# Kernel optimization log

Measured on AMD Instinct MI355X. Metric: run time of the kernel, lower is better.

## Reference

```python
import jax, jax.numpy as jnp
import numpy as np

N = 500_000      # nodes
E = 1_500_000    # edges (avg degree ~3, AIG-like)
F_IN = 4         # node feature dim
H = 32           # hidden dim fixed by module
S = 7            # state feature dim
BN_EPS = 1e-5


def setup_inputs():
    key = jax.random.key(0)
    ks = jax.random.split(key, 32)
    rn = lambda k, shape, s=0.1: jax.random.normal(k, shape, dtype=jnp.float32) * s
    inp = {}
    inp["states"] = rn(ks[0], (S,), 1.0)
    inp["x"] = rn(ks[1], (N, F_IN), 1.0)
    inp["edge_index"] = jax.random.randint(ks[2], (2, E), 0, N, dtype=jnp.int32)
    inp["edge_attr"] = rn(ks[3], (E, 1), 1.0)
    inp["batch"] = jnp.zeros((N,), dtype=jnp.int32)  # single graph
    dims = [F_IN, H, H]
    for i, (d, k0) in enumerate(zip(dims, [4, 10, 16]), start=1):
        inp[f"eps{i}"] = jnp.zeros((1,), jnp.float32)
        inp[f"elw{i}"] = rn(ks[k0], (d,))            # edge lin: Linear(1, d)
        inp[f"elb{i}"] = jnp.zeros((d,), jnp.float32)
        inp[f"w{i}"] = rn(ks[k0 + 1], (d, H))
        inp[f"b{i}"] = jnp.zeros((H,), jnp.float32)
        inp[f"g{i}"] = jnp.ones((H,), jnp.float32)   # BN gamma
        inp[f"bt{i}"] = jnp.zeros((H,), jnp.float32) # BN beta
    inp["sw"] = rn(ks[22], (S, 16))
    inp["sb"] = jnp.zeros((16,), jnp.float32)
    inp["a1w"] = rn(ks[23], (H + 16, H))
    inp["a1b"] = jnp.zeros((H,), jnp.float32)
    inp["a2w"] = rn(ks[24], (H, 6))
    inp["a2b"] = jnp.zeros((6,), jnp.float32)
    return inp


def _bn(h, g, b):
    # BatchNorm1d over node dim (training-mode batch statistics)
    mu = h.mean(0)
    var = h.var(0)
    return (h - mu) * jax.lax.rsqrt(var + BN_EPS) * g + b


def _gine(x, src, dst, edge_attr, eps, elw, elb, w, b, g, bt):
    # GINEConv: nn((1+eps)*x_i + sum_j relu(x_j + lin(e_ij)))
    e = edge_attr * elw[None, :] + elb                  # [E, d]
    m = jax.nn.relu(x[src] + e)                          # gather + edge-add + relu
    agg = jax.ops.segment_sum(m, dst, num_segments=x.shape[0])  # scatter-sum
    h = (1.0 + eps) * x + agg
    return jax.nn.relu(_bn(h @ w + b, g, bt))


def reference(states, x, edge_index, edge_attr, batch,
              eps1, elw1, elb1, w1, b1, g1, bt1,
              eps2, elw2, elb2, w2, b2, g2, bt2,
              eps3, elw3, elb3, w3, b3, g3, bt3,
              sw, sb, a1w, a1b, a2w, a2b):
    src, dst = edge_index[0], edge_index[1]
    h = _gine(x, src, dst, edge_attr, eps1, elw1, elb1, w1, b1, g1, bt1)
    h = _gine(h, src, dst, edge_attr, eps2, elw2, elb2, w2, b2, g2, bt2)
    h = _gine(h, src, dst, edge_attr, eps3, elw3, elb3, w3, b3, g3, bt3)
    # (global mean/max pooling in the torch forward only feeds the cached
    #  value-head input, not the returned actor output -> omitted here)
    state_x = jax.nn.relu(states @ sw + sb)              # [16]
    a = jnp.concatenate([h, jnp.broadcast_to(state_x, (h.shape[0], 16))], axis=1)
    a = jax.nn.relu(a @ a1w + a1b)
    logits = a @ a2w + a2b                               # [N, num_actions]
    return jax.nn.softmax(logits, axis=-1)               # global_softmax=False
```

## Files before the change

kernel.cpp:

```cpp
#include <hip/hip_runtime.h>
#include <hip/hip_fp16.h>
#include <math.h>

#define TPB 256
#define SCAN_CHUNK 1024
#define NBLK_LAYER 2048
#define NGROUPS (NBLK_LAYER * 8)
#define NBLK_TEAM 2048

struct alignas(16) half8 { __half h[8]; };

__global__ __launch_bounds__(256) void prep_kernel(
    const float* __restrict__ states, const float* __restrict__ sw,
    const float* __restrict__ sb, const float* __restrict__ a1w,
    const float* __restrict__ a1b, float* __restrict__ stats,
    float* __restrict__ c2, int zcount) {
  int t = threadIdx.x;
  for (int j = t; j < zcount; j += 256) stats[j] = 0.0f;
  __shared__ float sx[16];
  if (t < 16) {
    float acc = sb[t];
#pragma unroll
    for (int k = 0; k < 7; ++k) acc += states[k] * sw[k * 16 + t];
    sx[t] = fmaxf(acc, 0.0f);
  }
  __syncthreads();
  if (t < 32) {
    float acc = a1b[t];
#pragma unroll
    for (int k = 0; k < 16; ++k) acc += sx[k] * a1w[(32 + k) * 32 + t];
    c2[t] = acc;
  }
}

__global__ __launch_bounds__(256) void hist3_k(const int* __restrict__ dst,
                                               int* __restrict__ cnt, int E,
                                               int N) {
  int team = blockIdx.x & 7;
  int member = blockIdx.x >> 3;
  int n8 = (N + 7) >> 3;
  int lo = team * n8;
  int hi = lo + n8 < N ? lo + n8 : N;
  int stride = (NBLK_TEAM >> 3) * TPB;
  for (int e = member * TPB + threadIdx.x; e < E; e += stride) {
    int d = dst[e];
    if (d >= lo && d < hi) atomicAdd(&cnt[d], 1);
  }
}

__global__ __launch_bounds__(256) void scan1_k(const int* __restrict__ cnt,
                                               int* __restrict__ pre,
                                               int* __restrict__ bsum, int N) {
  __shared__ int lds[256];
  int b = blockIdx.x, t = threadIdx.x;
  int base = b * SCAN_CHUNK + t * 4;
  int c0 = (base + 0 < N) ? cnt[base + 0] : 0;
  int c1 = (base + 1 < N) ? cnt[base + 1] : 0;
  int c2 = (base + 2 < N) ? cnt[base + 2] : 0;
  int c3 = (base + 3 < N) ? cnt[base + 3] : 0;
  int s = c0 + c1 + c2 + c3;
  lds[t] = s;
  __syncthreads();
  int val = s;
  for (int off = 1; off < 256; off <<= 1) {
    int add = (t >= off) ? lds[t - off] : 0;
    __syncthreads();
    val += add;
    lds[t] = val;
    __syncthreads();
  }
  int excl = val - s;
  if (base + 0 < N) pre[base + 0] = excl;
  if (base + 1 < N) pre[base + 1] = excl + c0;
  if (base + 2 < N) pre[base + 2] = excl + c0 + c1;
  if (base + 3 < N) pre[base + 3] = excl + c0 + c1 + c2;
  if (t == 255) bsum[b] = val;
}

__global__ __launch_bounds__(512) void scan2_k(int* __restrict__ bsum, int nb) {
  __shared__ int lds[512];
  int t = threadIdx.x;
  int v = (t < nb) ? bsum[t] : 0;
  lds[t] = v;
  __syncthreads();
  int val = v;
  for (int off = 1; off < 512; off <<= 1) {
    int add = (t >= off) ? lds[t - off] : 0;
    __syncthreads();
    val += add;
    lds[t] = val;
    __syncthreads();
  }
  if (t < nb) bsum[t] = val - v;
}

__global__ __launch_bounds__(256) void scan3_k(int* __restrict__ pre,
                                               int* __restrict__ cursor,
                                               const int* __restrict__ bsum,
                                               int N, int E) {
  int i = blockIdx.x * TPB + threadIdx.x;
  if (i == 0) pre[N] = E;
  if (i >= N) return;
  int v = pre[i] + bsum[i >> 10];
  pre[i] = v;
  cursor[i] = v;
}

__global__ __launch_bounds__(256) void scatter3_k(
    const int* __restrict__ src, const int* __restrict__ dst,
    const float* __restrict__ ea, int* __restrict__ cursor,
    int2* __restrict__ pe, int E, int N) {
  int team = blockIdx.x & 7;
  int member = blockIdx.x >> 3;
  int n8 = (N + 7) >> 3;
  int lo = team * n8;
  int hi = lo + n8 < N ? lo + n8 : N;
  int stride = (NBLK_TEAM >> 3) * TPB;
  for (int e = member * TPB + threadIdx.x; e < E; e += stride) {
    int d = dst[e];
    if (d >= lo && d < hi) {
      int p = atomicAdd(&cursor[d], 1);
      pe[p] = make_int2(src[e], __float_as_int(ea[e]));
    }
  }
}

__global__ __launch_bounds__(256) void layer1_k(
    const int* __restrict__ rowptr, const int2* __restrict__ pe,
    const float* __restrict__ x, const float* __restrict__ elw,
    const float* __restrict__ elb, const float* __restrict__ w,
    const float* __restrict__ b, const float* __restrict__ epsp,
    __half* __restrict__ zh, float* __restrict__ ostats, int N) {
  const int tid = threadIdx.x;
  const int c = tid & 31;
  const int group0 = blockIdx.x * 8 + (tid >> 5);
  float wc0 = w[0 * 32 + c], wc1 = w[1 * 32 + c], wc2 = w[2 * 32 + c],
        wc3 = w[3 * 32 + c];
  float bc = b[c];
  float w0 = elw[0], w1 = elw[1], w2 = elw[2], w3 = elw[3];
  float e0 = elb[0], e1 = elb[1], e2 = elb[2], e3 = elb[3];
  float one_eps = 1.0f + epsp[0];
  float sl = 0.f, sq = 0.f;
  for (int i = group0; i < N; i += NGROUPS) {
    int p0 = rowptr[i], p1 = rowptr[i + 1];
    float a0 = 0.f, a1 = 0.f, a2 = 0.f, a3 = 0.f;
    for (int p = p0 + c; p < p1; p += 32) {
      int2 e = pe[p];
      float a = __int_as_float(e.y);
      float4 xv = *reinterpret_cast<const float4*>(x + (size_t)e.x * 4);
      a0 += fmaxf(xv.x + fmaf(a, w0, e0), 0.f);
      a1 += fmaxf(xv.y + fmaf(a, w1, e1), 0.f);
      a2 += fmaxf(xv.z + fmaf(a, w2, e2), 0.f);
      a3 += fmaxf(xv.w + fmaf(a, w3, e3), 0.f);
    }
#pragma unroll
    for (int off = 16; off; off >>= 1) {
      a0 += __shfl_xor(a0, off, 32);
      a1 += __shfl_xor(a1, off, 32);
      a2 += __shfl_xor(a2, off, 32);
      a3 += __shfl_xor(a3, off, 32);
    }
    float4 xv = *reinterpret_cast<const float4*>(x + (size_t)i * 4);
    float h0 = fmaf(one_eps, xv.x, a0);
    float h1 = fmaf(one_eps, xv.y, a1);
    float h2 = fmaf(one_eps, xv.z, a2);
    float h3 = fmaf(one_eps, xv.w, a3);
    float zv = bc;
    zv = fmaf(h0, wc0, zv);
    zv = fmaf(h1, wc1, zv);
    zv = fmaf(h2, wc2, zv);
    zv = fmaf(h3, wc3, zv);
    zh[(size_t)i * 32 + c] = __float2half(zv);
    sl += zv;
    sq = fmaf(zv, zv, sq);
  }
  __shared__ float rs[256], rq[256];
  rs[tid] = sl;
  rq[tid] = sq;
  __syncthreads();
  if (tid < 32) {
    float a = 0.f, qq = 0.f;
#pragma unroll
    for (int g = 0; g < 8; ++g) {
      a += rs[g * 32 + tid];
      qq += rq[g * 32 + tid];
    }
    int slot = blockIdx.x & 7;
    atomicAdd(&ostats[slot * 32 + tid], a);
    atomicAdd(&ostats[256 + slot * 32 + tid], qq);
  }
}

__global__ __launch_bounds__(256) void layerH_k(
    const int* __restrict__ rowptr, const int2* __restrict__ pe,
    const __half* __restrict__ zprev, const float* __restrict__ pstats,
    const float* __restrict__ pg, const float* __restrict__ pbt,
    const float* __restrict__ elw, const float* __restrict__ elb,
    const float* __restrict__ w, const float* __restrict__ b,
    const float* __restrict__ epsp, __half* __restrict__ zh,
    float* __restrict__ ostats, int N) {
  const int tid = threadIdx.x;
  const int c = tid & 31;
  const int gib = tid >> 5;
  const int group0 = blockIdx.x * 8 + gib;
  float ps = 0.f, pq = 0.f;
#pragma unroll
  for (int s = 0; s < 8; ++s) {
    ps += pstats[s * 32 + c];
    pq += pstats[256 + s * 32 + c];
  }
  float mu = ps / (float)N;
  float var = pq / (float)N - mu * mu;
  float scale = rsqrtf(var + 1e-5f) * pg[c];
  float shift = pbt[c] - mu * scale;
  float wcol[32];
#pragma unroll
  for (int k = 0; k < 32; ++k) wcol[k] = w[k * 32 + c];
  float elwc = elw[c], elbc = elb[c], bc = b[c];
  float one_eps = 1.0f + epsp[0];
  float sl = 0.f, sq = 0.f;
  __shared__ float hlds[256];
  for (int i = group0; i < N; i += NGROUPS) {
    int p0 = rowptr[i], p1 = rowptr[i + 1];
    float hself =
        fmaxf(fmaf(scale, __half2float(zprev[(size_t)i * 32 + c]), shift), 0.f);
    float acc = 0.f;
    for (int p = p0; p < p1; ++p) {
      int2 e = pe[p];
      float hs = fmaxf(
          fmaf(scale, __half2float(zprev[(size_t)e.x * 32 + c]), shift), 0.f);
      acc += fmaxf(hs + fmaf(__int_as_float(e.y), elwc, elbc), 0.f);
    }
    float hh = fmaf(one_eps, hself, acc);
    hlds[tid] = hh;
    float zv = bc;
    const float4* hp = reinterpret_cast<const float4*>(&hlds[gib * 32]);
#pragma unroll
    for (int kk = 0; kk < 8; ++kk) {
      float4 h4 = hp[kk];
      zv = fmaf(h4.x, wcol[kk * 4 + 0], zv);
      zv = fmaf(h4.y, wcol[kk * 4 + 1], zv);
      zv = fmaf(h4.z, wcol[kk * 4 + 2], zv);
      zv = fmaf(h4.w, wcol[kk * 4 + 3], zv);
    }
    zh[(size_t)i * 32 + c] = __float2half(zv);
    sl += zv;
    sq = fmaf(zv, zv, sq);
  }
  __shared__ float rs[256], rq[256];
  rs[tid] = sl;
  rq[tid] = sq;
  __syncthreads();
  if (tid < 32) {
    float a = 0.f, qq = 0.f;
#pragma unroll
    for (int g = 0; g < 8; ++g) {
      a += rs[g * 32 + tid];
      qq += rq[g * 32 + tid];
    }
    int slot = blockIdx.x & 7;
    atomicAdd(&ostats[slot * 32 + tid], a);
    atomicAdd(&ostats[256 + slot * 32 + tid], qq);
  }
}

__global__ __launch_bounds__(256) void head_k(
    const __half* __restrict__ zh, const float* __restrict__ pstats,
    const float* __restrict__ pg, const float* __restrict__ pbt,
    const float* __restrict__ a1w, const float* __restrict__ c2,
    const float* __restrict__ a2w, const float* __restrict__ a2b,
    float* __restrict__ out, int N) {
  const int tid = threadIdx.x;
  const int c = tid & 31;
  const int gib = tid >> 5;
  const int group0 = blockIdx.x * 8 + gib;
  float ps = 0.f, pq = 0.f;
#pragma unroll
  for (int s = 0; s < 8; ++s) {
    ps += pstats[s * 32 + c];
    pq += pstats[256 + s * 32 + c];
  }
  float mu = ps / (float)N;
  float var = pq / (float)N - mu * mu;
  float scale = rsqrtf(var + 1e-5f) * pg[c];
  float shift = pbt[c] - mu * scale;
  float wcol[32];
#pragma unroll
  for (int k = 0; k < 32; ++k) wcol[k] = a1w[k * 32 + c];
  float c2c = c2[c];
  const int j = c & 7;
  const int g = c >> 3;
  float w2r[8];
#pragma unroll
  for (int u = 0; u < 8; ++u)
    w2r[u] = (j < 6) ? a2w[(8 * g + u) * 6 + j] : 0.f;
  float bj = (j < 6) ? a2b[j] : 0.f;
  __shared__ float ylds[256];
  __shared__ float alds[256];
  __shared__ float llds[64];
  for (int i = group0; i < N; i += NGROUPS) {
    float y =
        fmaxf(fmaf(scale, __half2float(zh[(size_t)i * 32 + c]), shift), 0.f);
    ylds[tid] = y;
    float a1 = c2c;
    const float4* yp = reinterpret_cast<const float4*>(&ylds[gib * 32]);
#pragma unroll
    for (int kk = 0; kk < 8; ++kk) {
      float4 y4 = yp[kk];
      a1 = fmaf(y4.x, wcol[kk * 4 + 0], a1);
      a1 = fmaf(y4.y, wcol[kk * 4 + 1], a1);
      a1 = fmaf(y4.z, wcol[kk * 4 + 2], a1);
      a1 = fmaf(y4.w, wcol[kk * 4 + 3], a1);
    }
    a1 = fmaxf(a1, 0.f);
    alds[tid] = a1;
    const float4* ap =
        reinterpret_cast<const float4*>(&alds[gib * 32 + g * 8]);
    float4 a4a = ap[0];
    float4 a4b = ap[1];
    float l = a4a.x * w2r[0];
    l = fmaf(a4a.y, w2r[1], l);
    l = fmaf(a4a.z, w2r[2], l);
    l = fmaf(a4a.w, w2r[3], l);
    l = fmaf(a4b.x, w2r[4], l);
    l = fmaf(a4b.y, w2r[5], l);
    l = fmaf(a4b.z, w2r[6], l);
    l = fmaf(a4b.w, w2r[7], l);
    l += __shfl_xor(l, 8, 32);
    l += __shfl_xor(l, 16, 32);
    l += bj;
    llds[gib * 8 + j] = l;
    const float4* lp = reinterpret_cast<const float4*>(&llds[gib * 8]);
    float4 L0 = lp[0];
    float4 L1 = lp[1];
    float mx =
        fmaxf(fmaxf(fmaxf(L0.x, L0.y), fmaxf(L0.z, L0.w)), fmaxf(L1.x, L1.y));
    float e0 = __expf(L0.x - mx), e1 = __expf(L0.y - mx),
          e2 = __expf(L0.z - mx), e3 = __expf(L0.w - mx),
          e4 = __expf(L1.x - mx), e5 = __expf(L1.y - mx);
    float inv = 1.0f / (e0 + e1 + e2 + e3 + e4 + e5);
    if (c < 6) {
      float v = e0;
      v = (c == 1) ? e1 : v;
      v = (c == 2) ? e2 : v;
      v = (c == 3) ? e3 : v;
      v = (c == 4) ? e4 : v;
      v = (c == 5) ? e5 : v;
      out[(size_t)i * 6 + c] = v * inv;
    }
  }
}

__global__ __launch_bounds__(256) void edge_d4(
    const int* __restrict__ src, const int* __restrict__ dst,
    const float* __restrict__ ea, const float* __restrict__ x,
    const float* __restrict__ elw, const float* __restrict__ elb,
    float* __restrict__ agg, int E) {
  int e = blockIdx.x * TPB + threadIdx.x;
  if (e >= E) return;
  int s = src[e], d = dst[e];
  float a = ea[e];
  float4 xv = *reinterpret_cast<const float4*>(x + (size_t)s * 4);
  float m0 = fmaxf(xv.x + a * elw[0] + elb[0], 0.0f);
  float m1 = fmaxf(xv.y + a * elw[1] + elb[1], 0.0f);
  float m2 = fmaxf(xv.z + a * elw[2] + elb[2], 0.0f);
  float m3 = fmaxf(xv.w + a * elw[3] + elb[3], 0.0f);
  float* ap = agg + (size_t)d * 32;
  atomicAdd(ap + 0, m0);
  atomicAdd(ap + 1, m1);
  atomicAdd(ap + 2, m2);
  atomicAdd(ap + 3, m3);
}

__global__ __launch_bounds__(256) void edge_d32(
    const int* __restrict__ src, const int* __restrict__ dst,
    const float* __restrict__ ea, const float* __restrict__ x,
    const float* __restrict__ elw, const float* __restrict__ elb,
    float* __restrict__ agg, int E) {
  int tid = blockIdx.x * TPB + threadIdx.x;
  int e = tid >> 5;
  int c = tid & 31;
  if (e >= E) return;
  int s = src[e], d = dst[e];
  float a = ea[e];
  float m = fmaxf(x[(size_t)s * 32 + c] + a * elw[c] + elb[c], 0.0f);
  atomicAdd(agg + (size_t)d * 32 + c, m);
}

template <int DIN>
__global__ __launch_bounds__(256) void node_a(
    const float* __restrict__ x, float* aggz, const float* __restrict__ w,
    const float* __restrict__ b, const float* __restrict__ epsp,
    float* __restrict__ ssum, float* __restrict__ ssq, int N) {
  int i = blockIdx.x * TPB + threadIdx.x;
  float zv[32];
  if (i < N) {
    float one_eps = 1.0f + epsp[0];
    float h[DIN];
    if constexpr (DIN == 4) {
      float4 xv = *reinterpret_cast<const float4*>(x + (size_t)i * 4);
      float4 av = *reinterpret_cast<const float4*>(aggz + (size_t)i * 32);
      h[0] = one_eps * xv.x + av.x;
      h[1] = one_eps * xv.y + av.y;
      h[2] = one_eps * xv.z + av.z;
      h[3] = one_eps * xv.w + av.w;
    } else {
#pragma unroll
      for (int k0 = 0; k0 < 32; k0 += 4) {
        float4 xv = *reinterpret_cast<const float4*>(x + (size_t)i * 32 + k0);
        float4 av =
            *reinterpret_cast<const float4*>(aggz + (size_t)i * 32 + k0);
        h[k0 + 0] = one_eps * xv.x + av.x;
        h[k0 + 1] = one_eps * xv.y + av.y;
        h[k0 + 2] = one_eps * xv.z + av.z;
        h[k0 + 3] = one_eps * xv.w + av.w;
      }
    }
#pragma unroll
    for (int c = 0; c < 32; ++c) zv[c] = b[c];
#pragma unroll
    for (int k = 0; k < DIN; ++k)
#pragma unroll
      for (int c = 0; c < 32; ++c) zv[c] = fmaf(h[k], w[k * 32 + c], zv[c]);
#pragma unroll
    for (int c0 = 0; c0 < 32; c0 += 4) {
      float4 o = make_float4(zv[c0], zv[c0 + 1], zv[c0 + 2], zv[c0 + 3]);
      *reinterpret_cast<float4*>(aggz + (size_t)i * 32 + c0) = o;
    }
  } else {
#pragma unroll
    for (int c = 0; c < 32; ++c) zv[c] = 0.0f;
  }
  __shared__ float ls[32], lq[32];
  if (threadIdx.x < 32) {
    ls[threadIdx.x] = 0.0f;
    lq[threadIdx.x] = 0.0f;
  }
  __syncthreads();
#pragma unroll
  for (int c = 0; c < 32; ++c) {
    float v = zv[c];
    float q = zv[c] * zv[c];
#pragma unroll
    for (int off = 32; off > 0; off >>= 1) {
      v += __shfl_xor(v, off, 64);
      q += __shfl_xor(q, off, 64);
    }
    if ((threadIdx.x & 63) == 0) {
      atomicAdd(&ls[c], v);
      atomicAdd(&lq[c], q);
    }
  }
  __syncthreads();
  if (threadIdx.x < 32) {
    atomicAdd(&ssum[threadIdx.x], ls[threadIdx.x]);
    atomicAdd(&ssq[threadIdx.x], lq[threadIdx.x]);
  }
}

__global__ __launch_bounds__(256) void node_b(
    const float* __restrict__ z, const float* __restrict__ ssum,
    const float* __restrict__ ssq, const float* __restrict__ g,
    const float* __restrict__ bt, float* __restrict__ out, int N) {
  __shared__ float sscale[32], sshift[32];
  if (threadIdx.x < 32) {
    int c = threadIdx.x;
    float mu = ssum[c] / (float)N;
    float var = ssq[c] / (float)N - mu * mu;
    float inv = 1.0f / sqrtf(var + 1e-5f);
    float sc = inv * g[c];
    sscale[c] = sc;
    sshift[c] = bt[c] - mu * sc;
  }
  __syncthreads();
  int i = blockIdx.x * TPB + threadIdx.x;
  if (i >= N) return;
#pragma unroll
  for (int c0 = 0; c0 < 32; c0 += 4) {
    float4 zv = *reinterpret_cast<const float4*>(z + (size_t)i * 32 + c0);
    float4 o;
    o.x = fmaxf(zv.x * sscale[c0 + 0] + sshift[c0 + 0], 0.0f);
    o.y = fmaxf(zv.y * sscale[c0 + 1] + sshift[c0 + 1], 0.0f);
    o.z = fmaxf(zv.z * sscale[c0 + 2] + sshift[c0 + 2], 0.0f);
    o.w = fmaxf(zv.w * sscale[c0 + 3] + sshift[c0 + 3], 0.0f);
    *reinterpret_cast<float4*>(out + (size_t)i * 32 + c0) = o;
  }
}

__global__ __launch_bounds__(256) void node_b3_head(
    const float* __restrict__ z, const float* __restrict__ ssum,
    const float* __restrict__ ssq, const float* __restrict__ g,
    const float* __restrict__ bt, const float* __restrict__ a1w,
    const float* __restrict__ c2, const float* __restrict__ a2w,
    const float* __restrict__ a2b, float* __restrict__ out, int N) {
  __shared__ float sscale[32], sshift[32];
  if (threadIdx.x < 32) {
    int c = threadIdx.x;
    float mu = ssum[c] / (float)N;
    float var = ssq[c] / (float)N - mu * mu;
    float inv = 1.0f / sqrtf(var + 1e-5f);
    float sc = inv * g[c];
    sscale[c] = sc;
    sshift[c] = bt[c] - mu * sc;
  }
  __syncthreads();
  int i = blockIdx.x * TPB + threadIdx.x;
  if (i >= N) return;
  float y[32];
#pragma unroll
  for (int c0 = 0; c0 < 32; c0 += 4) {
    float4 zv = *reinterpret_cast<const float4*>(z + (size_t)i * 32 + c0);
    y[c0 + 0] = fmaxf(zv.x * sscale[c0 + 0] + sshift[c0 + 0], 0.0f);
    y[c0 + 1] = fmaxf(zv.y * sscale[c0 + 1] + sshift[c0 + 1], 0.0f);
    y[c0 + 2] = fmaxf(zv.z * sscale[c0 + 2] + sshift[c0 + 2], 0.0f);
    y[c0 + 3] = fmaxf(zv.w * sscale[c0 + 3] + sshift[c0 + 3], 0.0f);
  }
  float a1[32];
#pragma unroll
  for (int c = 0; c < 32; ++c) a1[c] = c2[c];
#pragma unroll
  for (int k = 0; k < 32; ++k)
#pragma unroll
    for (int c = 0; c < 32; ++c) a1[c] = fmaf(y[k], a1w[k * 32 + c], a1[c]);
#pragma unroll
  for (int c = 0; c < 32; ++c) a1[c] = fmaxf(a1[c], 0.0f);
  float lg[6];
#pragma unroll
  for (int j = 0; j < 6; ++j) lg[j] = a2b[j];
#pragma unroll
  for (int k = 0; k < 32; ++k)
#pragma unroll
    for (int j = 0; j < 6; ++j) lg[j] = fmaf(a1[k], a2w[k * 6 + j], lg[j]);
  float mx = lg[0];
#pragma unroll
  for (int j = 1; j < 6; ++j) mx = fmaxf(mx, lg[j]);
  float s = 0.0f;
#pragma unroll
  for (int j = 0; j < 6; ++j) {
    lg[j] = expf(lg[j] - mx);
    s += lg[j];
  }
  float rs = 1.0f / s;
#pragma unroll
  for (int j = 0; j < 6; ++j) out[(size_t)i * 6 + j] = lg[j] * rs;
}

extern "C" void kernel_launch(void* const* d_in, const int* in_sizes, int n_in,
                              void* d_out, int out_size, void* d_ws,
                              size_t ws_size, hipStream_t stream) {
  const float* states = (const float*)d_in[0];
  const float* x = (const float*)d_in[1];
  const int* ei = (const int*)d_in[2];
  const float* ea = (const float*)d_in[3];
  const float* eps1 = (const float*)d_in[5];
  const float* elw1 = (const float*)d_in[6];
  const float* elb1 = (const float*)d_in[7];
  const float* w1 = (const float*)d_in[8];
  const float* b1 = (const float*)d_in[9];
  const float* g1 = (const float*)d_in[10];
  const float* bt1 = (const float*)d_in[11];
  const float* eps2 = (const float*)d_in[12];
  const float* elw2 = (const float*)d_in[13];
  const float* elb2 = (const float*)d_in[14];
  const float* w2 = (const float*)d_in[15];
  const float* b2 = (const float*)d_in[16];
  const float* g2 = (const float*)d_in[17];
  const float* bt2 = (const float*)d_in[18];
  const float* eps3 = (const float*)d_in[19];
  const float* elw3 = (const float*)d_in[20];
  const float* elb3 = (const float*)d_in[21];
  const float* w3 = (const float*)d_in[22];
  const float* b3 = (const float*)d_in[23];
  const float* g3 = (const float*)d_in[24];
  const float* bt3 = (const float*)d_in[25];
  const float* sw = (const float*)d_in[26];
  const float* sb = (const float*)d_in[27];
  const float* a1w = (const float*)d_in[28];
  const float* a1b = (const float*)d_in[29];
  const float* a2w = (const float*)d_in[30];
  const float* a2b = (const float*)d_in[31];

  int N = in_sizes[1] / 4;
  int E = in_sizes[3];
  const int* src = ei;
  const int* dst = ei + E;
  float* out = (float*)d_out;

  char* wsb = (char*)d_ws;
  __half* zhA = (__half*)wsb;
  __half* zhB = (__half*)(wsb + (size_t)64 * N);
  float* stats = (float*)(wsb + (size_t)128 * N);
  float* c2csr = stats + 1536;
  int2* pe = (int2*)(c2csr + 32);
  int* rowptr = (int*)(pe + (size_t)E);
  int* cursor = rowptr + (N + 1);
  int* bsum = cursor + N;

  int nblkN = (N + TPB - 1) / TPB;
  int nblkE = (E + TPB - 1) / TPB;
  int nb = (N + SCAN_CHUNK - 1) / SCAN_CHUNK;

  size_t need = (size_t)128 * N + 6272 + (size_t)8 * E + (size_t)4 * (N + 1) +
                (size_t)4 * N + 2048;

  if (ws_size >= need && nb <= 512) {
    prep_kernel<<<1, TPB, 0, stream>>>(states, sw, sb, a1w, a1b, stats, c2csr,
                                       1536);
    hipMemsetAsync(cursor, 0, (size_t)N * sizeof(int), stream);
    hist3_k<<<NBLK_TEAM, TPB, 0, stream>>>(dst, cursor, E, N);
    scan1_k<<<nb, TPB, 0, stream>>>(cursor, rowptr, bsum, N);
    scan2_k<<<1, 512, 0, stream>>>(bsum, nb);
    scan3_k<<<nblkN, TPB, 0, stream>>>(rowptr, cursor, bsum, N, E);
    scatter3_k<<<NBLK_TEAM, TPB, 0, stream>>>(src, dst, ea, cursor, pe, E, N);

    layer1_k<<<NBLK_LAYER, TPB, 0, stream>>>(rowptr, pe, x, elw1, elb1, w1, b1,
                                             eps1, zhA, stats + 0, N);
    layerH_k<<<NBLK_LAYER, TPB, 0, stream>>>(rowptr, pe, zhA, stats + 0, g1,
                                             bt1, elw2, elb2, w2, b2, eps2,
                                             zhB, stats + 512, N);
    layerH_k<<<NBLK_LAYER, TPB, 0, stream>>>(rowptr, pe, zhB, stats + 512, g2,
                                             bt2, elw3, elb3, w3, b3, eps3,
                                             zhA, stats + 1024, N);
    head_k<<<NBLK_LAYER, TPB, 0, stream>>>(zhA, stats + 1024, g3, bt3, a1w,
                                           c2csr, a2w, a2b, out, N);
  } else {
    float* zA = (float*)d_ws;
    float* zB = zA + (size_t)N * 32;
    float* statsFB = zB + (size_t)N * 32;
    float* c2fb = statsFB + 192;
    prep_kernel<<<1, TPB, 0, stream>>>(states, sw, sb, a1w, a1b, statsFB, c2fb,
                                       192);
    size_t aggBytes = (size_t)N * 32 * sizeof(float);
    int nblkE32 = (int)(((long long)E * 32 + TPB - 1) / TPB);
    hipMemsetAsync(zA, 0, aggBytes, stream);
    edge_d4<<<nblkE, TPB, 0, stream>>>(src, dst, ea, x, elw1, elb1, zA, E);
    node_a<4><<<nblkN, TPB, 0, stream>>>(x, zA, w1, b1, eps1, statsFB + 0,
                                         statsFB + 32, N);
    node_b<<<nblkN, TPB, 0, stream>>>(zA, statsFB + 0, statsFB + 32, g1, bt1,
                                      zB, N);
    hipMemsetAsync(zA, 0, aggBytes, stream);
    edge_d32<<<nblkE32, TPB, 0, stream>>>(src, dst, ea, zB, elw2, elb2, zA, E);
    node_a<32><<<nblkN, TPB, 0, stream>>>(zB, zA, w2, b2, eps2, statsFB + 64,
                                          statsFB + 96, N);
    node_b<<<nblkN, TPB, 0, stream>>>(zA, statsFB + 64, statsFB + 96, g2, bt2,
                                      zB, N);
    hipMemsetAsync(zA, 0, aggBytes, stream);
    edge_d32<<<nblkE32, TPB, 0, stream>>>(src, dst, ea, zB, elw3, elb3, zA, E);
    node_a<32><<<nblkN, TPB, 0, stream>>>(zB, zA, w3, b3, eps3, statsFB + 128,
                                          statsFB + 160, N);
    node_b3_head<<<nblkN, TPB, 0, stream>>>(zA, statsFB + 128, statsFB + 160,
                                            g3, bt3, a1w, c2fb, a2w, a2b, out,
                                            N);
  }
}
```

Before: 485.6 us.

## Remap layerH gather to 16 lanes per node with half2 channel pairs

Reworks the hidden-layer GINE kernel so each 64-lane wave handles 4 nodes at once, with 16 lanes per node each gathering two channels through a half2 load. The edge loop then runs for 4 nodes in parallel per wave instead of 2 per 64 lanes, which targets per-node latency and divergence across rows of different degree. The 32x32 matmul is then done by remapping lanes so each half-wave computes two nodes from LDS. BN scale and shift are now computed once per block into shared memory. The cost is an extra LDS round trip, an added barrier, and divergence between the 4 node groups in a wave when their degrees differ.

```diff
diff --git a/kernel.cpp b/kernel.cpp
--- a/kernel.cpp
+++ b/kernel.cpp
@@ -200,52 +200,87 @@
     const float* __restrict__ epsp, __half* __restrict__ zh,
     float* __restrict__ ostats, int N) {
   const int tid = threadIdx.x;
-  const int c = tid & 31;
-  const int gib = tid >> 5;
-  const int group0 = blockIdx.x * 8 + gib;
-  float ps = 0.f, pq = 0.f;
-#pragma unroll
-  for (int s = 0; s < 8; ++s) {
-    ps += pstats[s * 32 + c];
-    pq += pstats[256 + s * 32 + c];
-  }
-  float mu = ps / (float)N;
-  float var = pq / (float)N - mu * mu;
-  float scale = rsqrtf(var + 1e-5f) * pg[c];
-  float shift = pbt[c] - mu * scale;
+  const int lane = tid & 63;
+  const int wid = tid >> 6;
+  const int g16 = lane >> 4;
+  const int c16 = lane & 15;
+  const int c = lane & 31;
+  const int half = lane >> 5;
+
+  __shared__ float sscale[32], sshift[32];
+  if (tid < 32) {
+    float ps = 0.f, pq = 0.f;
+#pragma unroll
+    for (int s = 0; s < 8; ++s) {
+      ps += pstats[s * 32 + tid];
+      pq += pstats[256 + s * 32 + tid];
+    }
+    float mu = ps / (float)N;
+    float var = pq / (float)N - mu * mu;
+    float sc = rsqrtf(var + 1e-5f) * pg[tid];
+    sscale[tid] = sc;
+    sshift[tid] = pbt[tid] - mu * sc;
+  }
+  __syncthreads();
+  const int ch0 = 2 * c16, ch1 = ch0 + 1;
+  const float scA = sscale[ch0], shA = sshift[ch0];
+  const float scB = sscale[ch1], shB = sshift[ch1];
+  const float ew0 = elw[ch0], eb0 = elb[ch0];
+  const float ew1 = elw[ch1], eb1 = elb[ch1];
   float wcol[32];
 #pragma unroll
   for (int k = 0; k < 32; ++k) wcol[k] = w[k * 32 + c];
-  float elwc = elw[c], elbc = elb[c], bc = b[c];
-  float one_eps = 1.0f + epsp[0];
+  const float bc = b[c];
+  const float one_eps = 1.0f + epsp[0];
   float sl = 0.f, sq = 0.f;
-  __shared__ float hlds[256];
-  for (int i = group0; i < N; i += NGROUPS) {
-    int p0 = rowptr[i], p1 = rowptr[i + 1];
-    float hself =
-        fmaxf(fmaf(scale, __half2float(zprev[(size_t)i * 32 + c]), shift), 0.f);
-    float acc = 0.f;
-    for (int p = p0; p < p1; ++p) {
-      int2 e = pe[p];
-      float hs = fmaxf(
-          fmaf(scale, __half2float(zprev[(size_t)e.x * 32 + c]), shift), 0.f);
-      acc += fmaxf(hs + fmaf(__int_as_float(e.y), elwc, elbc), 0.f);
-    }
-    float hh = fmaf(one_eps, hself, acc);
-    hlds[tid] = hh;
-    float zv = bc;
-    const float4* hp = reinterpret_cast<const float4*>(&hlds[gib * 32]);
-#pragma unroll
-    for (int kk = 0; kk < 8; ++kk) {
-      float4 h4 = hp[kk];
-      zv = fmaf(h4.x, wcol[kk * 4 + 0], zv);
-      zv = fmaf(h4.y, wcol[kk * 4 + 1], zv);
-      zv = fmaf(h4.z, wcol[kk * 4 + 2], zv);
-      zv = fmaf(h4.w, wcol[kk * 4 + 3], zv);
-    }
-    zh[(size_t)i * 32 + c] = __float2half(zv);
-    sl += zv;
-    sq = fmaf(zv, zv, sq);
+  __shared__ float hlds[4][4][32];
+  const int waveBase = (blockIdx.x * 4 + wid) * 4;
+  const int STRIDE = NBLK_LAYER * 16;
+  for (int iBase = waveBase; iBase < N; iBase += STRIDE) {
+    const int i = iBase + g16;
+    const bool valid = i < N;
+    float hh0 = 0.f, hh1 = 0.f;
+    if (valid) {
+      int p0 = rowptr[i], p1 = rowptr[i + 1];
+      __half2 zs =
+          *reinterpret_cast<const __half2*>(zprev + (size_t)i * 32 + ch0);
+      float hs0 = fmaxf(fmaf(scA, __half2float(zs.x), shA), 0.f);
+      float hs1 = fmaxf(fmaf(scB, __half2float(zs.y), shB), 0.f);
+      float acc0 = 0.f, acc1 = 0.f;
+      for (int p = p0; p < p1; ++p) {
+        int2 e = pe[p];
+        __half2 hz =
+            *reinterpret_cast<const __half2*>(zprev + (size_t)e.x * 32 + ch0);
+        float eaf = __int_as_float(e.y);
+        float t0 = fmaxf(fmaf(scA, __half2float(hz.x), shA), 0.f);
+        float t1 = fmaxf(fmaf(scB, __half2float(hz.y), shB), 0.f);
+        acc0 += fmaxf(t0 + fmaf(eaf, ew0, eb0), 0.f);
+        acc1 += fmaxf(t1 + fmaf(eaf, ew1, eb1), 0.f);
+      }
+      hh0 = fmaf(one_eps, hs0, acc0);
+      hh1 = fmaf(one_eps, hs1, acc1);
+    }
+    *reinterpret_cast<float2*>(&hlds[wid][g16][ch0]) = make_float2(hh0, hh1);
+#pragma unroll
+    for (int u = 0; u < 2; ++u) {
+      int nn = 2 * half + u;
+      int inode = iBase + nn;
+      if (inode < N) {
+        float zv = bc;
+        const float4* hp = reinterpret_cast<const float4*>(&hlds[wid][nn][0]);
+#pragma unroll
+        for (int kk = 0; kk < 8; ++kk) {
+          float4 h4 = hp[kk];
+          zv = fmaf(h4.x, wcol[kk * 4 + 0], zv);
+          zv = fmaf(h4.y, wcol[kk * 4 + 1], zv);
+          zv = fmaf(h4.z, wcol[kk * 4 + 2], zv);
+          zv = fmaf(h4.w, wcol[kk * 4 + 3], zv);
+        }
+        zh[(size_t)inode * 32 + c] = __float2half(zv);
+        sl += zv;
+        sq = fmaf(zv, zv, sq);
+      }
+    }
   }
   __shared__ float rs[256], rq[256];
   rs[tid] = sl;
```

New measurement: 528.8 us. 1.09x slower.
